# Performance work log

Measured on AMD Instinct MI355X. Metric: run time of the kernel, lower is better.

## Reference

```python
import jax, jax.numpy as jnp
import numpy as np

S, B, LAG, H, F = 10, 16384, 5, 512, 5

def setup_inputs() -> dict:
    key = jax.random.key(0)
    ks = jax.random.split(key, 16)
    sc = 0.05
    inp = {
        'x': jax.random.normal(ks[0], (S, B, LAG), jnp.float32),
        'W_in': jax.random.normal(ks[1], (H, LAG), jnp.float32) * sc,
        'b_in': jax.random.normal(ks[2], (H,), jnp.float32) * sc,
        'Wih0': jax.random.normal(ks[3], (4 * H, H), jnp.float32) * sc,
        'Whh0': jax.random.normal(ks[4], (4 * H, H), jnp.float32) * sc,
        'bih0': jax.random.normal(ks[5], (4 * H,), jnp.float32) * sc,
        'bhh0': jax.random.normal(ks[6], (4 * H,), jnp.float32) * sc,
        'Wih1': jax.random.normal(ks[7], (4 * H, H), jnp.float32) * sc,
        'Whh1': jax.random.normal(ks[8], (4 * H, H), jnp.float32) * sc,
        'bih1': jax.random.normal(ks[9], (4 * H,), jnp.float32) * sc,
        'bhh1': jax.random.normal(ks[10], (4 * H,), jnp.float32) * sc,
        'W_out': jax.random.normal(ks[11], (1, H), jnp.float32) * sc,
        'b_out': jax.random.normal(ks[12], (1,), jnp.float32) * sc,
        'W_f': jax.random.normal(ks[13], (F, H), jnp.float32) * sc,
        'b_f': jax.random.normal(ks[14], (F,), jnp.float32) * sc,
    }
    return inp

def _lstm_cell(g, h, c, Whh, bhh):
    # g: precomputed input-side gates [B,4H]; add recurrent part, PyTorch gate order i,f,g,o
    g = g + h @ Whh.T + bhh
    i, f, gg, o = jnp.split(g, 4, axis=-1)
    c_new = jax.nn.sigmoid(f) * c + jax.nn.sigmoid(i) * jnp.tanh(gg)
    h_new = jax.nn.sigmoid(o) * jnp.tanh(c_new)
    return h_new, c_new

def reference(x, W_in, b_in, Wih0, Whh0, bih0, bhh0, Wih1, Whh1, bih1, bhh1, W_out, b_out, W_f, b_f):
    # input projection for all steps at once: [S,B,H]
    u = x @ W_in.T + b_in
    # precompute input-side LSTM gates for layer 0: [S,B,4H]
    g0_all = u @ Wih0.T + bih0
    zeros = jnp.zeros((B, H), x.dtype)

    def step(carry, g0_t):
        h0, c0, h1, c1 = carry
        h0, c0 = _lstm_cell(g0_t, h0, c0, Whh0, bhh0)
        g1 = h0 @ Wih1.T + bih1  # dropout between layers is eval-mode no-op
        h1, c1 = _lstm_cell(g1, h1, c1, Whh1, bhh1)
        return (h0, c0, h1, c1), h1

    (h0, c0, h1, c1), hs = jax.lax.scan(step, (zeros, zeros, zeros, zeros), g0_all)
    # per-step scalar outputs: [S,B,1] -> [B,S]
    step_out = (hs @ W_out.T + b_out)[:, :, 0].T
    # forecast head from last layer's final hidden state: [B,F]
    fc = h1 @ W_f.T + b_f
    outputs = jnp.concatenate([step_out, fc], axis=1)  # [B, S+F]
    h_n = jnp.stack([h0, h1])  # [2,B,H]
    c_n = jnp.stack([c0, c1])
    return outputs, h_n, c_n
```

## Files before the change

kernel.cpp:

```cpp
#include <hip/hip_runtime.h>
#include <hip/hip_bf16.h>

constexpr int S   = 10;
constexpr int Bsz = 16384;
constexpr int LAG = 5;
constexpr int H   = 512;
constexpr int G4  = 4 * H;
constexpr int F   = 5;
constexpr int BH  = Bsz * H;
constexpr int OUT_HN = Bsz * (S + F);
constexpr int OUT_CN = OUT_HN + 2 * BH;

constexpr int TK   = 32;
constexpr int NBUF = 3;
constexpr int BM   = 256;
constexpr int BNR  = 128;
constexpr int A_T  = BM  * TK;
constexpr int B_T  = BNR * TK;

typedef __attribute__((ext_vector_type(8))) short short8;
typedef __attribute__((ext_vector_type(4))) float f32x4;

template <int I> struct Int { static constexpr int val = I; };

template <int N, typename F>
__device__ __forceinline__ void static_for(F&& f) {
    if constexpr (N > 0) {
        static_for<N - 1>(f);
        f(Int<N - 1>{});
    }
}

__device__ __forceinline__ float sigf(float x) { return 1.0f / (1.0f + __expf(-x)); }
__device__ __forceinline__ float tanh_fast(float x) {
    float e = __expf(2.0f * x);
    return 1.0f - 2.0f / (e + 1.0f);
}

__device__ __forceinline__ void gload_lds16(const void* g, void* l) {
    __builtin_amdgcn_global_load_lds(
        (const __attribute__((address_space(1))) unsigned int*)g,
        (__attribute__((address_space(3))) unsigned int*)l, 16, 0, 0);
}

__global__ __launch_bounds__(256)
void prep_kernel(const float* __restrict__ W_in,  const float* __restrict__ b_in,
                 const float* __restrict__ Wih0,  const float* __restrict__ Whh0,
                 const float* __restrict__ bih0,  const float* __restrict__ bhh0,
                 const float* __restrict__ Wih1,  const float* __restrict__ Whh1,
                 const float* __restrict__ bih1,  const float* __restrict__ bhh1,
                 __hip_bfloat16* __restrict__ W0b, __hip_bfloat16* __restrict__ W1b,
                 float* __restrict__ A0r, float* __restrict__ b0r,
                 float* __restrict__ b1r)
{
    const int r   = blockIdx.x;
    const int tid = threadIdx.x;

    for (int k = tid; k < H; k += 256)
        W0b[r * H + k] = __float2bfloat16(Whh0[r * H + k]);
    for (int k = tid; k < 2 * H; k += 256)
        W1b[r * 2 * H + k] = __float2bfloat16(
            (k < H) ? Wih1[r * H + k] : Whh1[r * H + (k - H)]);

    if (tid < LAG) {
        float s = 0.f;
        for (int h = 0; h < H; ++h) s += Wih0[r * H + h] * W_in[h * LAG + tid];
        A0r[r * LAG + tid] = s;
    } else if (tid == 5) {
        float s = 0.f;
        for (int h = 0; h < H; ++h) s += Wih0[r * H + h] * b_in[h];
        b0r[r] = s + bih0[r] + bhh0[r];
    } else if (tid == 6) {
        b1r[r] = bih1[r] + bhh1[r];
    }
}

template <int NT>
__global__ __launch_bounds__(512, 4)
void lstm_gemm(const __hip_bfloat16* __restrict__ A,
               const __hip_bfloat16* __restrict__ W, int ldw,
               const float* __restrict__ bias,
               const float* __restrict__ xs,
               const float* __restrict__ A0r,
               const float* __restrict__ c_in,
               float* __restrict__ c_out,
               float* __restrict__ h32_out,
               __hip_bfloat16* __restrict__ hb16_out,
               int hcol)
{
    __shared__ __align__(16) short As[NBUF * A_T];
    __shared__ __align__(16) short Bs[NBUF * B_T];
    __shared__ float xls[BM * LAG];
    __shared__ float a0ls[BNR * LAG];

    const int tid  = threadIdx.x;
    const int lane = tid & 63;
    const int quad = lane >> 4;
    const int li   = lane & 15;
    const int wv   = tid >> 6;
    const int wy   = wv >> 1;
    const int wx   = wv & 1;

    const int l  = blockIdx.y * gridDim.x + blockIdx.x;
    const int v  = (l & 7) * 128 + (l >> 3);
    const int by = v >> 4;
    const int bx = v & 15;
    const int bM_ = by * BM;
    const int cn  = bx * 32;

    const bool has_x = (xs != nullptr);
    if (has_x) {
        for (int i = tid; i < BM * LAG; i += 512) {
            const int row = i / LAG, ll = i % LAG;
            xls[i] = xs[(size_t)(bM_ + row) * LAG + ll];
        }
        for (int i = tid; i < BNR * LAG; i += 512) {
            const int cl = i / LAG, ll = i % LAG;
            const int r  = (cl >> 5) * H + cn + (cl & 31);
            a0ls[i] = A0r[r * LAG + ll];
        }
        __syncthreads();
    }

    f32x4 acc[4][4];
    #pragma unroll
    for (int i = 0; i < 4; ++i)
        #pragma unroll
        for (int j = 0; j < 4; ++j) acc[i][j] = (f32x4){0.f, 0.f, 0.f, 0.f};

    if constexpr (NT > 0) {
        const short* Ab = (const short*)A;
        const short* Wb = (const short*)W;
        int a_off0, a_off1, w_off;
        {
            const int row0 = tid >> 2, j0 = tid & 3;
            a_off0 = (bM_ + row0) * 1024 + (j0 ^ ((row0 >> 1) & 3)) * 8;
            const int idx1 = 512 + tid;
            const int row1 = idx1 >> 2, j1 = idx1 & 3;
            a_off1 = (bM_ + row1) * 1024 + (j1 ^ ((row1 >> 1) & 3)) * 8;
            const int rw = tid >> 2, jw = tid & 3;
            const int rr = (rw >> 5) * H + cn + (rw & 31);
            w_off = rr * ldw + (jw ^ ((rw >> 1) & 3)) * 8;
        }
        const int adst0 = tid * 8;
        const int adst1 = (512 + tid) * 8;
        const int bdst  = tid * 8;

        auto stage = [&](auto tc) {
            constexpr int t   = decltype(tc)::val;
            constexpr int buf = t % NBUF;
            gload_lds16(Ab + t * TK + a_off0, &As[buf * A_T + adst0]);
            gload_lds16(Ab + t * TK + a_off1, &As[buf * A_T + adst1]);
            gload_lds16(Wb + t * TK + w_off,  &Bs[buf * B_T + bdst]);
        };

        const int pch = quad ^ ((li >> 1) & 3);
        const int arow = (wy * 64 + li) * TK + pch * 8;
        const int brow = (wx * 16 + li) * TK + pch * 8;

        stage(Int<0>{});
        stage(Int<1>{});

        static_for<NT>([&](auto tc) {
            constexpr int t   = decltype(tc)::val;
            constexpr int buf = t % NBUF;
            if constexpr (t + 1 < NT)
                asm volatile("s_waitcnt vmcnt(3)\n\ts_barrier" ::: "memory");
            else
                asm volatile("s_waitcnt vmcnt(0)\n\ts_barrier" ::: "memory");

            const short* as = As + buf * A_T;
            const short* bs = Bs + buf * B_T;
            short8 af[4], bf[4];
            #pragma unroll
            for (int m = 0; m < 4; ++m)
                af[m] = *(const short8*)&as[arow + m * 16 * TK];
            #pragma unroll
            for (int g = 0; g < 4; ++g)
                bf[g] = *(const short8*)&bs[brow + g * 32 * TK];

            if constexpr (t + 2 < NT) stage(Int<t + 2>{});

            __builtin_amdgcn_s_setprio(1);
            #pragma unroll
            for (int m = 0; m < 4; ++m)
                #pragma unroll
                for (int g = 0; g < 4; ++g)
                    acc[m][g] = __builtin_amdgcn_mfma_f32_16x16x32_bf16(
                        af[m], bf[g], acc[m][g], 0, 0, 0);
            __builtin_amdgcn_s_setprio(0);
        });
    }

    const int n = cn + wx * 16 + li;
    float bias4[4], a0reg[4][LAG];
    #pragma unroll
    for (int g = 0; g < 4; ++g) bias4[g] = bias[g * H + n];
    if (has_x) {
        #pragma unroll
        for (int g = 0; g < 4; ++g)
            #pragma unroll
            for (int ll = 0; ll < LAG; ++ll)
                a0reg[g][ll] = a0ls[(g * 32 + wx * 16 + li) * LAG + ll];
    }

    #pragma unroll
    for (int mt = 0; mt < 4; ++mt) {
        #pragma unroll
        for (int reg = 0; reg < 4; ++reg) {
            const int b_loc = wy * 64 + mt * 16 + quad * 4 + reg;
            const int b     = bM_ + b_loc;
            float g4[4];
            #pragma unroll
            for (int g = 0; g < 4; ++g) g4[g] = acc[mt][g][reg] + bias4[g];
            if (has_x) {
                #pragma unroll
                for (int ll = 0; ll < LAG; ++ll) {
                    const float xv = xls[b_loc * LAG + ll];
                    #pragma unroll
                    for (int g = 0; g < 4; ++g) g4[g] = fmaf(xv, a0reg[g][ll], g4[g]);
                }
            }
            const float ig = sigf(g4[0]);
            const float fg = sigf(g4[1]);
            const float gg = tanh_fast(g4[2]);
            const float og = sigf(g4[3]);
            const float cold = c_in ? c_in[(size_t)b * H + n] : 0.f;
            const float cnew = fg * cold + ig * gg;
            const float hh   = og * tanh_fast(cnew);
            c_out[(size_t)b * H + n] = cnew;
            if (h32_out) h32_out[(size_t)b * H + n] = hh;
            hb16_out[(size_t)b * 1024 + hcol + n] = __float2bfloat16(hh);
        }
    }
}

__global__ __launch_bounds__(256)
void out_head(const __hip_bfloat16* __restrict__ hcat,
              const float* __restrict__ W_out, const float* __restrict__ b_out,
              const float* __restrict__ W_f,   const float* __restrict__ b_f,
              float* __restrict__ out, int s, int last)
{
    const int wave = threadIdx.x >> 6;
    const int lane = threadIdx.x & 63;
    const int b    = blockIdx.x * 4 + wave;

    const __hip_bfloat16* hrow = hcat + (size_t)b * 1024 + 512;
    short8 hv = *(const short8*)&hrow[lane * 8];
    float h8[8];
    #pragma unroll
    for (int i = 0; i < 8; ++i) {
        union { unsigned int u; float f; } cv;
        cv.u = ((unsigned int)(unsigned short)hv[i]) << 16;
        h8[i] = cv.f;
    }

    {
        const float4 w0 = *reinterpret_cast<const float4*>(&W_out[lane * 8]);
        const float4 w1 = *reinterpret_cast<const float4*>(&W_out[lane * 8 + 4]);
        const float w8[8] = {w0.x, w0.y, w0.z, w0.w, w1.x, w1.y, w1.z, w1.w};
        float v = 0.f;
        #pragma unroll
        for (int i = 0; i < 8; ++i) v = fmaf(h8[i], w8[i], v);
        #pragma unroll
        for (int off = 32; off > 0; off >>= 1) v += __shfl_down(v, off, 64);
        if (lane == 0) out[b * (S + F) + s] = v + b_out[0];
    }
    if (last) {
        for (int f = 0; f < F; ++f) {
            const float4 w0 = *reinterpret_cast<const float4*>(&W_f[f * H + lane * 8]);
            const float4 w1 = *reinterpret_cast<const float4*>(&W_f[f * H + lane * 8 + 4]);
            const float w8[8] = {w0.x, w0.y, w0.z, w0.w, w1.x, w1.y, w1.z, w1.w};
            float v = 0.f;
            #pragma unroll
            for (int i = 0; i < 8; ++i) v = fmaf(h8[i], w8[i], v);
            #pragma unroll
            for (int off = 32; off > 0; off >>= 1) v += __shfl_down(v, off, 64);
            if (lane == 0) out[b * (S + F) + S + f] = v + b_f[f];
        }
    }
}

extern "C" void kernel_launch(void* const* d_in, const int* in_sizes, int n_in,
                              void* d_out, int out_size, void* d_ws, size_t ws_size,
                              hipStream_t stream)
{
    const float* x     = (const float*)d_in[0];
    const float* W_in  = (const float*)d_in[1];
    const float* b_in  = (const float*)d_in[2];
    const float* Wih0  = (const float*)d_in[3];
    const float* Whh0  = (const float*)d_in[4];
    const float* bih0  = (const float*)d_in[5];
    const float* bhh0  = (const float*)d_in[6];
    const float* Wih1  = (const float*)d_in[7];
    const float* Whh1  = (const float*)d_in[8];
    const float* bih1  = (const float*)d_in[9];
    const float* bhh1  = (const float*)d_in[10];
    const float* W_out = (const float*)d_in[11];
    const float* b_out = (const float*)d_in[12];
    const float* W_f   = (const float*)d_in[13];
    const float* b_f   = (const float*)d_in[14];

    float* out = (float*)d_out;
    char*  ws  = (char*)d_ws;

    __hip_bfloat16* hcat0 = (__hip_bfloat16*)ws;
    __hip_bfloat16* hcat1 = hcat0 + (size_t)Bsz * 1024;
    __hip_bfloat16* W0b   = hcat1 + (size_t)Bsz * 1024;
    __hip_bfloat16* W1b   = W0b + (size_t)G4 * H;
    float* A0r = (float*)(W1b + (size_t)G4 * 2 * H);
    float* b0r = A0r + G4 * LAG;
    float* b1r = b0r + G4;

    float* hn0 = out + OUT_HN;
    float* hn1 = out + OUT_HN + BH;
    float* c0  = out + OUT_CN;
    float* c1  = out + OUT_CN + BH;

    prep_kernel<<<dim3(G4), dim3(256), 0, stream>>>(
        W_in, b_in, Wih0, Whh0, bih0, bhh0, Wih1, Whh1, bih1, bhh1,
        W0b, W1b, A0r, b0r, b1r);

    __hip_bfloat16* hbuf[2] = {hcat0, hcat1};
    const dim3 grid(16, 64);
    const dim3 blk(512);

    for (int s = 0; s < S; ++s) {
        const bool first = (s == 0);
        const bool last  = (s == S - 1);
        __hip_bfloat16* cur = hbuf[s & 1];
        __hip_bfloat16* nxt = hbuf[(s + 1) & 1];

        if (first)
            lstm_gemm<0><<<grid, blk, 0, stream>>>(
                nullptr, W0b, H, b0r,
                x + (size_t)s * Bsz * LAG, A0r,
                nullptr, c0, nullptr, cur, 0);
        else
            lstm_gemm<16><<<grid, blk, 0, stream>>>(
                nxt, W0b, H, b0r,
                x + (size_t)s * Bsz * LAG, A0r,
                c0, c0, last ? hn0 : nullptr, cur, 0);

        if (first)
            lstm_gemm<16><<<grid, blk, 0, stream>>>(
                cur, W1b, 2 * H, b1r,
                nullptr, nullptr,
                nullptr, c1, nullptr, nxt, H);
        else
            lstm_gemm<32><<<grid, blk, 0, stream>>>(
                cur, W1b, 2 * H, b1r,
                nullptr, nullptr,
                c1, c1, last ? hn1 : nullptr, nxt, H);

        out_head<<<dim3(Bsz / 4), dim3(256), 0, stream>>>(
            nxt, W_out, b_out, W_f, b_f, out, s, last ? 1 : 0);
    }
}
```

Baseline: 1.651 ms.

## Pre-swizzle weights into MFMA fragment layout and load B directly to registers

```diff
diff --git a/kernel.cpp b/kernel.cpp
--- a/kernel.cpp
+++ b/kernel.cpp
@@ -15,16 +15,15 @@
 constexpr int NBUF = 3;
 constexpr int BM   = 256;
 constexpr int BNR  = 128;
-constexpr int A_T  = BM  * TK;
-constexpr int B_T  = BNR * TK;
+constexpr int A_T  = BM * TK;
 
 typedef __attribute__((ext_vector_type(8))) short short8;
 typedef __attribute__((ext_vector_type(4))) float f32x4;
 
 template <int I> struct Int { static constexpr int val = I; };
 
-template <int N, typename F>
-__device__ __forceinline__ void static_for(F&& f) {
+template <int N, typename Fn>
+__device__ __forceinline__ void static_for(Fn&& f) {
     if constexpr (N > 0) {
         static_for<N - 1>(f);
         f(Int<N - 1>{});
@@ -49,18 +48,34 @@
                  const float* __restrict__ bih0,  const float* __restrict__ bhh0,
                  const float* __restrict__ Wih1,  const float* __restrict__ Whh1,
                  const float* __restrict__ bih1,  const float* __restrict__ bhh1,
-                 __hip_bfloat16* __restrict__ W0b, __hip_bfloat16* __restrict__ W1b,
+                 __hip_bfloat16* __restrict__ W0f, __hip_bfloat16* __restrict__ W1f,
                  float* __restrict__ A0r, float* __restrict__ b0r,
                  float* __restrict__ b1r)
 {
     const int r   = blockIdx.x;
     const int tid = threadIdx.x;
 
-    for (int k = tid; k < H; k += 256)
-        W0b[r * H + k] = __float2bfloat16(Whh0[r * H + k]);
-    for (int k = tid; k < 2 * H; k += 256)
-        W1b[r * 2 * H + k] = __float2bfloat16(
-            (k < H) ? Wih1[r * H + k] : Whh1[r * H + (k - H)]);
+    const int g  = r >> 9;
+    const int u  = r & 511;
+    const int bx = u >> 5;
+    const int wx = (u >> 4) & 1;
+    const int li = u & 15;
+
+    for (int k = tid; k < H; k += 256) {
+        const int t = k >> 5, quad = (k >> 3) & 3, e = k & 7;
+        const int lane = quad * 16 + li;
+        const size_t dst = ((size_t)(bx * 16 + t) * 8 + g * 2 + wx) * 512
+                         + lane * 8 + e;
+        W0f[dst] = __float2bfloat16(Whh0[r * H + k]);
+    }
+    for (int k = tid; k < 2 * H; k += 256) {
+        const int t = k >> 5, quad = (k >> 3) & 3, e = k & 7;
+        const int lane = quad * 16 + li;
+        const size_t dst = ((size_t)(bx * 32 + t) * 8 + g * 2 + wx) * 512
+                         + lane * 8 + e;
+        const float src = (k < H) ? Wih1[r * H + k] : Whh1[r * H + (k - H)];
+        W1f[dst] = __float2bfloat16(src);
+    }
 
     if (tid < LAG) {
         float s = 0.f;
@@ -75,10 +90,10 @@
     }
 }
 
-template <int NT>
+template <int NT, int NTW>
 __global__ __launch_bounds__(512, 4)
 void lstm_gemm(const __hip_bfloat16* __restrict__ A,
-               const __hip_bfloat16* __restrict__ W, int ldw,
+               const __hip_bfloat16* __restrict__ Wf,
                const float* __restrict__ bias,
                const float* __restrict__ xs,
                const float* __restrict__ A0r,
@@ -89,7 +104,6 @@
                int hcol)
 {
     __shared__ __align__(16) short As[NBUF * A_T];
-    __shared__ __align__(16) short Bs[NBUF * B_T];
     __shared__ float xls[BM * LAG];
     __shared__ float a0ls[BNR * LAG];
 
@@ -130,64 +144,81 @@
 
     if constexpr (NT > 0) {
         const short* Ab = (const short*)A;
-        const short* Wb = (const short*)W;
-        int a_off0, a_off1, w_off;
+        int a_off0, a_off1;
         {
             const int row0 = tid >> 2, j0 = tid & 3;
             a_off0 = (bM_ + row0) * 1024 + (j0 ^ ((row0 >> 1) & 3)) * 8;
             const int idx1 = 512 + tid;
             const int row1 = idx1 >> 2, j1 = idx1 & 3;
             a_off1 = (bM_ + row1) * 1024 + (j1 ^ ((row1 >> 1) & 3)) * 8;
-            const int rw = tid >> 2, jw = tid & 3;
-            const int rr = (rw >> 5) * H + cn + (rw & 31);
-            w_off = rr * ldw + (jw ^ ((rw >> 1) & 3)) * 8;
         }
         const int adst0 = tid * 8;
         const int adst1 = (512 + tid) * 8;
-        const int bdst  = tid * 8;
-
-        auto stage = [&](auto tc) {
+
+        auto stageA = [&](auto tc) {
             constexpr int t   = decltype(tc)::val;
             constexpr int buf = t % NBUF;
             gload_lds16(Ab + t * TK + a_off0, &As[buf * A_T + adst0]);
             gload_lds16(Ab + t * TK + a_off1, &As[buf * A_T + adst1]);
-            gload_lds16(Wb + t * TK + w_off,  &Bs[buf * B_T + bdst]);
         };
 
-        const int pch = quad ^ ((li >> 1) & 3);
+        const short* wf = (const short*)Wf + (size_t)bx * NTW * 8 * 512
+                        + wx * 512 + lane * 8;
+
+        const int pch  = quad ^ ((li >> 1) & 3);
         const int arow = (wy * 64 + li) * TK + pch * 8;
-        const int brow = (wx * 16 + li) * TK + pch * 8;
-
-        stage(Int<0>{});
-        stage(Int<1>{});
+
+        short8 bf[2][4];
+
+        stageA(Int<0>{});
+        #pragma unroll
+        for (int g = 0; g < 4; ++g)
+            bf[0][g] = *(const short8*)&wf[(g * 2) * 512];
+        stageA(Int<1>{});
 
         static_for<NT>([&](auto tc) {
             constexpr int t   = decltype(tc)::val;
             constexpr int buf = t % NBUF;
+            constexpr int cb  = t & 1;
             if constexpr (t + 1 < NT)
-                asm volatile("s_waitcnt vmcnt(3)\n\ts_barrier" ::: "memory");
+                asm volatile("s_waitcnt vmcnt(2)\n\ts_barrier" ::: "memory");
             else
                 asm volatile("s_waitcnt vmcnt(0)\n\ts_barrier" ::: "memory");
 
             const short* as = As + buf * A_T;
-            const short* bs = Bs + buf * B_T;
-            short8 af[4], bf[4];
-            #pragma unroll
-            for (int m = 0; m < 4; ++m)
-                af[m] = *(const short8*)&as[arow + m * 16 * TK];
-            #pragma unroll
-            for (int g = 0; g < 4; ++g)
-                bf[g] = *(const short8*)&bs[brow + g * 32 * TK];
-
-            if constexpr (t + 2 < NT) stage(Int<t + 2>{});
-
-            __builtin_amdgcn_s_setprio(1);
-            #pragma unroll
-            for (int m = 0; m < 4; ++m)
+            short8 af0 = *(const short8*)&as[arow + 0 * 16 * TK];
+            short8 af1 = *(const short8*)&as[arow + 1 * 16 * TK];
+
+            if constexpr (t + 1 < NT) {
                 #pragma unroll
                 for (int g = 0; g < 4; ++g)
-                    acc[m][g] = __builtin_amdgcn_mfma_f32_16x16x32_bf16(
-                        af[m], bf[g], acc[m][g], 0, 0, 0);
+                    bf[cb ^ 1][g] =
+                        *(const short8*)&wf[((t + 1) * 8 + g * 2) * 512];
+            }
+            if constexpr (t + 2 < NT) stageA(Int<t + 2>{});
+
+            __builtin_amdgcn_s_setprio(1);
+            #pragma unroll
+            for (int g = 0; g < 4; ++g)
+                acc[0][g] = __builtin_amdgcn_mfma_f32_16x16x32_bf16(
+                    af0, bf[cb][g], acc[0][g], 0, 0, 0);
+            #pragma unroll
+            for (int g = 0; g < 4; ++g)
+                acc[1][g] = __builtin_amdgcn_mfma_f32_16x16x32_bf16(
+                    af1, bf[cb][g], acc[1][g], 0, 0, 0);
+            __builtin_amdgcn_s_setprio(0);
+
+            short8 af2 = *(const short8*)&as[arow + 2 * 16 * TK];
+            short8 af3 = *(const short8*)&as[arow + 3 * 16 * TK];
+            __builtin_amdgcn_s_setprio(1);
+            #pragma unroll
+            for (int g = 0; g < 4; ++g)
+                acc[2][g] = __builtin_amdgcn_mfma_f32_16x16x32_bf16(
+                    af2, bf[cb][g], acc[2][g], 0, 0, 0);
+            #pragma unroll
+            for (int g = 0; g < 4; ++g)
+                acc[3][g] = __builtin_amdgcn_mfma_f32_16x16x32_bf16(
+                    af3, bf[cb][g], acc[3][g], 0, 0, 0);
             __builtin_amdgcn_s_setprio(0);
         });
     }
@@ -306,9 +337,9 @@
 
     __hip_bfloat16* hcat0 = (__hip_bfloat16*)ws;
     __hip_bfloat16* hcat1 = hcat0 + (size_t)Bsz * 1024;
-    __hip_bfloat16* W0b   = hcat1 + (size_t)Bsz * 1024;
-    __hip_bfloat16* W1b   = W0b + (size_t)G4 * H;
-    float* A0r = (float*)(W1b + (size_t)G4 * 2 * H);
+    __hip_bfloat16* W0f   = hcat1 + (size_t)Bsz * 1024;
+    __hip_bfloat16* W1f   = W0f + (size_t)G4 * H;
+    float* A0r = (float*)(W1f + (size_t)G4 * 2 * H);
     float* b0r = A0r + G4 * LAG;
     float* b1r = b0r + G4;
 
@@ -319,7 +350,7 @@
 
     prep_kernel<<<dim3(G4), dim3(256), 0, stream>>>(
         W_in, b_in, Wih0, Whh0, bih0, bhh0, Wih1, Whh1, bih1, bhh1,
-        W0b, W1b, A0r, b0r, b1r);
+        W0f, W1f, A0r, b0r, b1r);
 
     __hip_bfloat16* hbuf[2] = {hcat0, hcat1};
     const dim3 grid(16, 64);
@@ -332,24 +363,24 @@
         __hip_bfloat16* nxt = hbuf[(s + 1) & 1];
 
         if (first)
-            lstm_gemm<0><<<grid, blk, 0, stream>>>(
-                nullptr, W0b, H, b0r,
+            lstm_gemm<0, 16><<<grid, blk, 0, stream>>>(
+                nullptr, W0f, b0r,
                 x + (size_t)s * Bsz * LAG, A0r,
                 nullptr, c0, nullptr, cur, 0);
         else
-            lstm_gemm<16><<<grid, blk, 0, stream>>>(
-                nxt, W0b, H, b0r,
+            lstm_gemm<16, 16><<<grid, blk, 0, stream>>>(
+                nxt, W0f, b0r,
                 x + (size_t)s * Bsz * LAG, A0r,
                 c0, c0, last ? hn0 : nullptr, cur, 0);
 
         if (first)
-            lstm_gemm<16><<<grid, blk, 0, stream>>>(
-                cur, W1b, 2 * H, b1r,
+            lstm_gemm<16, 32><<<grid, blk, 0, stream>>>(
+                cur, W1f, b1r,
                 nullptr, nullptr,
                 nullptr, c1, nullptr, nxt, H);
         else
-            lstm_gemm<32><<<grid, blk, 0, stream>>>(
-                cur, W1b, 2 * H, b1r,
+            lstm_gemm<32, 32><<<grid, blk, 0, stream>>>(
+                cur, W1f, b1r,
                 nullptr, nullptr,
                 c1, c1, last ? hn1 : nullptr, nxt, H);
 
```

After: 1.731 ms. 1.05x slower.
